# Optimization experiments

Measured on AMD Instinct MI355X. Metric: run time of the kernel, lower is better.

## Reference

```python
import jax, jax.numpy as jnp
import numpy as np

N = 524288   # total graph nodes
V = 64       # number of virtual nodes (clusters)
C = N // V   # nodes per cluster (8192)
D = 256      # in_feats
H = 256      # hidden_feats
EPS = 1e-5


def setup_inputs() -> dict:
    key = jax.random.key(0)
    ks = jax.random.split(key, 8)
    sD = 1.0 / np.sqrt(D)
    sH = 1.0 / np.sqrt(2 * H)
    inp = {
        "x": jax.random.normal(ks[0], (N, D), dtype=jnp.float32),
        "vn_emb": jax.random.normal(ks[1], (V, D), dtype=jnp.float32) * 0.1,
        "wq": jax.random.normal(ks[2], (D, D), dtype=jnp.float32) * sD,
        "wk": jax.random.normal(ks[3], (D, D), dtype=jnp.float32) * sD,
        "v_attn": jax.random.normal(ks[4], (D,), dtype=jnp.float32) * sD,
        "w1": jax.random.normal(ks[5], (D, 2 * H), dtype=jnp.float32) * sD,
        "b1": jnp.zeros((2 * H,), dtype=jnp.float32),
        "g1": jnp.ones((2 * H,), dtype=jnp.float32),
        "beta1": jnp.zeros((2 * H,), dtype=jnp.float32),
        "w2": jax.random.normal(ks[6], (2 * H, H), dtype=jnp.float32) * sH,
        "b2": jnp.zeros((H,), dtype=jnp.float32),
        "g2": jnp.ones((H,), dtype=jnp.float32),
        "beta2": jnp.zeros((H,), dtype=jnp.float32),
        # cluster v owns contiguous node block [v*C, (v+1)*C)
        "vn_index": jnp.arange(N, dtype=jnp.int32).reshape(V, C),
        "vn_indices": jnp.stack(
            [jnp.arange(N, dtype=jnp.int32), (jnp.arange(N, dtype=jnp.int32) // C)],
            axis=1),
    }
    return inp


def _batchnorm(z, g, b):
    # training-mode BN over the virtual-node batch dim
    m = jnp.mean(z, axis=0)
    v = jnp.var(z, axis=0)
    return (z - m) * jax.lax.rsqrt(v + EPS) * g + b


def reference(x, vn_emb, wq, wk, v_attn, w1, b1, g1, beta1,
              w2, b2, g2, beta2, vn_index, vn_indices):
    vx = vn_emb                                   # [V, D]
    # --- update_node_emb (layer 0): broadcast-add VN emb to its nodes ---
    h = x + vx[vn_indices[:, 1]]                  # [N, D]
    # --- update_vn_emb: per-cluster additive attention pooling (vectorized over V) ---
    cluster_h = h[vn_index]                       # [V, C, D]
    q = vx @ wq                                   # [V, D]
    kproj = jnp.einsum('vcd,de->vce', cluster_h, wk)   # [V, C, D]
    scores = jnp.einsum('vce,e->vc', jnp.tanh(kproj + q[:, None, :]), v_attn)
    attn = jax.nn.softmax(scores, axis=-1)        # [V, C]
    pooled = jnp.einsum('vc,vcd->vd', attn, cluster_h) + vx  # [V, D]
    # --- mlp_vns[0]: Linear -> BN -> ReLU -> Linear -> BN -> ReLU ---
    z = jax.nn.relu(_batchnorm(pooled @ w1 + b1, g1, beta1))  # [V, 2H]
    vx_new = jax.nn.relu(_batchnorm(z @ w2 + b2, g2, beta2))  # [V, H]
    return h, vx_new
```

## Files before the change

### kernel.cpp

```cpp
#include <hip/hip_runtime.h>


typedef __bf16 bf16x8 __attribute__((ext_vector_type(8)));
typedef float f32x4 __attribute__((ext_vector_type(4)));
typedef unsigned short us8 __attribute__((ext_vector_type(8)));

__device__ __forceinline__ unsigned short f2bf(float f) {
  unsigned int u = __float_as_uint(f);
  return (unsigned short)((u + 0x7fffu + ((u >> 16) & 1u)) >> 16);
}
__device__ __forceinline__ float bf2f(unsigned short s) {
  return __uint_as_float(((unsigned int)s) << 16);
}
__device__ __forceinline__ float tanh_fast(float x) {
  float cx = fminf(fmaxf(x, -15.f), 15.f);
  float e = __expf(2.f * cx);
  return (e - 1.f) * __builtin_amdgcn_rcpf(e + 1.f);
}
__device__ __forceinline__ float wave_sum(float v) {
#pragma unroll
  for (int o = 1; o < 64; o <<= 1) v += __shfl_xor(v, o);
  return v;
}
__device__ __forceinline__ void lgkm_barrier() {
  asm volatile("s_waitcnt lgkmcnt(0)" ::: "memory");
  __builtin_amdgcn_sched_barrier(0);
  __builtin_amdgcn_s_barrier();
  __builtin_amdgcn_sched_barrier(0);
}

__global__ __launch_bounds__(256) void k_prep(
    const float* __restrict__ vn_emb, const float* __restrict__ wq,
    const float* __restrict__ wk, float* __restrict__ qg,
    unsigned short* __restrict__ wkp) {
  int t = threadIdx.x;
  int b = blockIdx.x;
  if (b < 64) {
    float a = 0.f;
#pragma unroll 4
    for (int d = 0; d < 256; ++d) a += vn_emb[(b << 8) + d] * wq[(d << 8) + t];
    qg[(b << 8) + t] = a;
  } else {
    int tid = ((b - 64) << 8) + t;
    int l = tid & 63;
    int ks = (tid >> 6) & 7;
    int ct = tid >> 9;
    int col = (ct << 4) + (l & 15);
    int d0 = (ks << 5) + ((l >> 4) << 3);
    us8 o;
#pragma unroll
    for (int e = 0; e < 8; ++e) o[e] = f2bf(wk[(d0 + e) * 256 + col]);
    *reinterpret_cast<us8*>(wkp + (size_t)tid * 8) = o;
  }
}

__global__ __launch_bounds__(256, 4) void k_main(
    const float* __restrict__ x, const float* __restrict__ vn_emb,
    const float* __restrict__ v_attn, const float* __restrict__ qg,
    const unsigned short* __restrict__ wkp, float* __restrict__ hout,
    float* __restrict__ vecs, float* __restrict__ Zb) {
  __shared__ unsigned short hs[64 * 256];
  __shared__ float vxs[256], qv[256], va[256];

  const int t = threadIdx.x;
  const int blk = blockIdx.x;
  const int cl = blk >> 4;

  vxs[t] = vn_emb[(cl << 8) + t];
  qv[t] = qg[(cl << 8) + t];
  va[t] = v_attn[t];
  __syncthreads();

  const int l = t & 63, wv = t >> 6;
  const int lr = l & 15, lg = l >> 4;

  const float4* xv = reinterpret_cast<const float4*>(x);
  float4* ho = reinterpret_cast<float4*>(hout);
  char* hsb = reinterpret_cast<char*>(hs);
  const size_t base = (size_t)blk << 15;

  f32x4 acc = {0.f, 0.f, 0.f, 0.f};
  float zacc = 0.f;

  for (int sub = 0; sub < 8; ++sub) {
    const size_t sbase = base + ((size_t)sub << 12);

#pragma unroll 8
    for (int i = 0; i < 16; ++i) {
      int id = (i << 8) + t;
      float4 xx = xv[sbase + id];
      int row = id >> 6;
      int c4 = id & 63;
      const float4 vv = *reinterpret_cast<const float4*>(&vxs[c4 << 2]);
      float4 hh;
      hh.x = xx.x + vv.x;
      hh.y = xx.y + vv.y;
      hh.z = xx.z + vv.z;
      hh.w = xx.w + vv.w;
      ho[sbase + id] = hh;
      ushort4 o;
      o.x = f2bf(hh.x);
      o.y = f2bf(hh.y);
      o.z = f2bf(hh.z);
      o.w = f2bf(hh.w);
      int boff = (row << 9) + (((c4 << 3)) ^ ((row & 7) << 4));
      *reinterpret_cast<ushort4*>(hsb + boff) = o;
    }
    lgkm_barrier();

    bf16x8 bfr[8];
    {
      int row = (wv << 4) + lr;
      int sw = (row & 7) << 4;
#pragma unroll
      for (int ks = 0; ks < 8; ++ks) {
        int boff = (row << 9) + (((ks << 6) + (lg << 4)) ^ sw);
        bfr[ks] = __builtin_bit_cast(
            bf16x8, *reinterpret_cast<const us8*>(hsb + boff));
      }
    }
    float sp = 0.f;
    for (int ct = 0; ct < 16; ++ct) {
      f32x4 ac0 = {0.f, 0.f, 0.f, 0.f};
#pragma unroll
      for (int ks = 0; ks < 8; ++ks) {
        bf16x8 af = __builtin_bit_cast(
            bf16x8, *reinterpret_cast<const us8*>(
                        wkp + ((size_t)(((ct << 3) + ks) << 6) + l) * 8));
        ac0 =
            __builtin_amdgcn_mfma_f32_16x16x32_bf16(af, bfr[ks], ac0, 0, 0, 0);
      }
      const int eo0 = (ct << 4) + (lg << 2);
#pragma unroll
      for (int r = 0; r < 4; ++r)
        sp += tanh_fast(ac0[r] + qv[eo0 + r]) * va[eo0 + r];
    }
    sp += __shfl_xor(sp, 16);
    sp += __shfl_xor(sp, 32);
    float wgt = __expf(sp);
    zacc += wgt;

#pragma unroll
    for (int n = 0; n < 16; ++n) {
      float wn = __shfl(wgt, n);
      int row = (wv << 4) + n;
      int boff = (row << 9) + (((l << 3)) ^ ((row & 7) << 4));
      ushort4 hv = *reinterpret_cast<const ushort4*>(hsb + boff);
      acc[0] += wn * bf2f(hv.x);
      acc[1] += wn * bf2f(hv.y);
      acc[2] += wn * bf2f(hv.z);
      acc[3] += wn * bf2f(hv.w);
    }
    lgkm_barrier();
  }

  float zsum = wave_sum(zacc) * 0.25f;
  if (l == 0) va[wv] = zsum;
  float* sc = reinterpret_cast<float*>(hs);
  *reinterpret_cast<f32x4*>(&sc[(wv << 8) + (l << 2)]) = acc;
  __syncthreads();
  vecs[((size_t)blk << 8) + t] =
      sc[t] + sc[256 + t] + sc[512 + t] + sc[768 + t];
  if (t == 0) Zb[blk] = va[0] + va[1] + va[2] + va[3];
}

__global__ __launch_bounds__(256) void k_combine(
    const float* __restrict__ vecs, const float* __restrict__ Zb,
    const float* __restrict__ vn_emb, float* __restrict__ pooledT) {
  int v = blockIdx.x, t = threadIdx.x;
  float s = 0.f, z = 0.f;
#pragma unroll
  for (int b = 0; b < 16; ++b) {
    s += vecs[(size_t)(((v << 4) + b) << 8) + t];
    z += Zb[(v << 4) + b];
  }
  pooledT[(t << 6) + v] = s / z + vn_emb[(v << 8) + t];
}

__global__ __launch_bounds__(64) void k_mlp1(
    const float* __restrict__ pooledT, const float* __restrict__ w1,
    const float* __restrict__ b1, const float* __restrict__ g1,
    const float* __restrict__ be1, float* __restrict__ z1T) {
  int j = blockIdx.x, v = threadIdx.x;
  float a = 0.f;
#pragma unroll 4
  for (int d = 0; d < 256; ++d) a += pooledT[(d << 6) + v] * w1[(d << 9) + j];
  a += b1[j];
  float mu = wave_sum(a) * (1.f / 64.f);
  float df = a - mu;
  float var = wave_sum(df * df) * (1.f / 64.f);
  float z = df * rsqrtf(var + 1e-5f) * g1[j] + be1[j];
  z1T[(j << 6) + v] = fmaxf(z, 0.f);
}

__global__ __launch_bounds__(64) void k_mlp2(
    const float* __restrict__ z1T, const float* __restrict__ w2,
    const float* __restrict__ b2, const float* __restrict__ g2,
    const float* __restrict__ be2, float* __restrict__ vout) {
  int j = blockIdx.x, v = threadIdx.x;
  float a = 0.f;
#pragma unroll 4
  for (int k = 0; k < 512; ++k) a += z1T[(k << 6) + v] * w2[(k << 8) + j];
  a += b2[j];
  float mu = wave_sum(a) * (1.f / 64.f);
  float df = a - mu;
  float var = wave_sum(df * df) * (1.f / 64.f);
  float z = df * rsqrtf(var + 1e-5f) * g2[j] + be2[j];
  vout[(v << 8) + j] = fmaxf(z, 0.f);
}

extern "C" void kernel_launch(void* const* d_in, const int* in_sizes, int n_in,
                              void* d_out, int out_size, void* d_ws,
                              size_t ws_size, hipStream_t stream) {
  const float* x = (const float*)d_in[0];
  const float* vn_emb = (const float*)d_in[1];
  const float* wq = (const float*)d_in[2];
  const float* wk = (const float*)d_in[3];
  const float* v_attn = (const float*)d_in[4];
  const float* w1 = (const float*)d_in[5];
  const float* b1 = (const float*)d_in[6];
  const float* g1 = (const float*)d_in[7];
  const float* beta1 = (const float*)d_in[8];
  const float* w2 = (const float*)d_in[9];
  const float* b2 = (const float*)d_in[10];
  const float* g2 = (const float*)d_in[11];
  const float* beta2 = (const float*)d_in[12];

  char* wsb = (char*)d_ws;
  float* qg = (float*)(wsb + 0);
  unsigned short* wkp = (unsigned short*)(wsb + 65536);
  float* vecs = (float*)(wsb + 196608);
  float* Zb = (float*)(wsb + 1245184);
  float* pooledT = (float*)(wsb + 1249280);
  float* z1T = (float*)(wsb + 1314816);

  float* hout = (float*)d_out;
  float* vout = hout + (size_t)524288 * 256;

  k_prep<<<96, 256, 0, stream>>>(vn_emb, wq, wk, qg, wkp);
  k_main<<<1024, 256, 0, stream>>>(x, vn_emb, v_attn, qg, wkp, hout, vecs, Zb);
  k_combine<<<64, 256, 0, stream>>>(vecs, Zb, vn_emb, pooledT);
  k_mlp1<<<512, 64, 0, stream>>>(pooledT, w1, b1, g1, beta1, z1T);
  k_mlp2<<<256, 64, 0, stream>>>(z1T, w2, b2, g2, beta2, vout);
}
```

Before: 389.8 us.

## Give each wave a private LDS tile to drop block barriers in main loop

After: 539.0 us. +38.3%, slower.

```diff
diff --git a/kernel.cpp b/kernel.cpp
--- a/kernel.cpp
+++ b/kernel.cpp
@@ -21,12 +21,6 @@
 #pragma unroll
   for (int o = 1; o < 64; o <<= 1) v += __shfl_xor(v, o);
   return v;
-}
-__device__ __forceinline__ void lgkm_barrier() {
-  asm volatile("s_waitcnt lgkmcnt(0)" ::: "memory");
-  __builtin_amdgcn_sched_barrier(0);
-  __builtin_amdgcn_s_barrier();
-  __builtin_amdgcn_sched_barrier(0);
 }
 
 __global__ __launch_bounds__(256) void k_prep(
@@ -54,12 +48,12 @@
   }
 }
 
-__global__ __launch_bounds__(256, 4) void k_main(
+__global__ __launch_bounds__(256, 3) void k_hs(
     const float* __restrict__ x, const float* __restrict__ vn_emb,
     const float* __restrict__ v_attn, const float* __restrict__ qg,
     const unsigned short* __restrict__ wkp, float* __restrict__ hout,
     float* __restrict__ vecs, float* __restrict__ Zb) {
-  __shared__ unsigned short hs[64 * 256];
+  __shared__ unsigned short hs[4][16 * 256];
   __shared__ float vxs[256], qv[256], va[256];
 
   const int t = threadIdx.x;
@@ -74,93 +68,85 @@
   const int l = t & 63, wv = t >> 6;
   const int lr = l & 15, lg = l >> 4;
 
-  const float4* xv = reinterpret_cast<const float4*>(x);
-  float4* ho = reinterpret_cast<float4*>(hout);
-  char* hsb = reinterpret_cast<char*>(hs);
-  const size_t base = (size_t)blk << 15;
+  char* myhs = reinterpret_cast<char*>(hs[wv]);
+  const f32x4 vv = *reinterpret_cast<const f32x4*>(&vxs[l << 2]);
 
   f32x4 acc = {0.f, 0.f, 0.f, 0.f};
   float zacc = 0.f;
 
-  for (int sub = 0; sub < 8; ++sub) {
-    const size_t sbase = base + ((size_t)sub << 12);
-
-#pragma unroll 8
+  const size_t wrow0 = ((size_t)blk << 9) + ((size_t)wv << 7);
+
+  for (int chunk = 0; chunk < 8; ++chunk) {
+    const size_t row0 = wrow0 + ((size_t)chunk << 4);
+
+#pragma unroll
     for (int i = 0; i < 16; ++i) {
-      int id = (i << 8) + t;
-      float4 xx = xv[sbase + id];
-      int row = id >> 6;
-      int c4 = id & 63;
-      const float4 vv = *reinterpret_cast<const float4*>(&vxs[c4 << 2]);
-      float4 hh;
-      hh.x = xx.x + vv.x;
-      hh.y = xx.y + vv.y;
-      hh.z = xx.z + vv.z;
-      hh.w = xx.w + vv.w;
-      ho[sbase + id] = hh;
+      const size_t gidx = ((row0 + i) << 8) + (l << 2);
+      f32x4 xr = *reinterpret_cast<const f32x4*>(&x[gidx]);
+      f32x4 hh = xr + vv;
+      *reinterpret_cast<f32x4*>(&hout[gidx]) = hh;
       ushort4 o;
-      o.x = f2bf(hh.x);
-      o.y = f2bf(hh.y);
-      o.z = f2bf(hh.z);
-      o.w = f2bf(hh.w);
-      int boff = (row << 9) + (((c4 << 3)) ^ ((row & 7) << 4));
-      *reinterpret_cast<ushort4*>(hsb + boff) = o;
-    }
-    lgkm_barrier();
+      o.x = f2bf(hh[0]);
+      o.y = f2bf(hh[1]);
+      o.z = f2bf(hh[2]);
+      o.w = f2bf(hh[3]);
+      *reinterpret_cast<ushort4*>(
+          myhs + ((i << 9) + ((l << 3) ^ ((i & 7) << 4)))) = o;
+    }
+    asm volatile("s_waitcnt lgkmcnt(0)" ::: "memory");
+    __builtin_amdgcn_sched_barrier(0);
 
     bf16x8 bfr[8];
     {
-      int row = (wv << 4) + lr;
-      int sw = (row & 7) << 4;
-#pragma unroll
-      for (int ks = 0; ks < 8; ++ks) {
-        int boff = (row << 9) + (((ks << 6) + (lg << 4)) ^ sw);
+      const int sw = (lr & 7) << 4;
+#pragma unroll
+      for (int ks = 0; ks < 8; ++ks)
         bfr[ks] = __builtin_bit_cast(
-            bf16x8, *reinterpret_cast<const us8*>(hsb + boff));
-      }
-    }
+            bf16x8, *reinterpret_cast<const us8*>(
+                        myhs + ((lr << 9) + ((((ks << 6) + (lg << 4))) ^ sw))));
+    }
+
     float sp = 0.f;
+#pragma unroll 4
     for (int ct = 0; ct < 16; ++ct) {
       f32x4 ac0 = {0.f, 0.f, 0.f, 0.f};
 #pragma unroll
       for (int ks = 0; ks < 8; ++ks) {
         bf16x8 af = __builtin_bit_cast(
             bf16x8, *reinterpret_cast<const us8*>(
-                        wkp + ((size_t)(((ct << 3) + ks) << 6) + l) * 8));
-        ac0 =
-            __builtin_amdgcn_mfma_f32_16x16x32_bf16(af, bfr[ks], ac0, 0, 0, 0);
+                        wkp + ((size_t)((((ct << 3) + ks) << 6) + l)) * 8));
+        ac0 = __builtin_amdgcn_mfma_f32_16x16x32_bf16(af, bfr[ks], ac0, 0, 0, 0);
       }
       const int eo0 = (ct << 4) + (lg << 2);
-#pragma unroll
-      for (int r = 0; r < 4; ++r)
-        sp += tanh_fast(ac0[r] + qv[eo0 + r]) * va[eo0 + r];
+      const f32x4 qf = *reinterpret_cast<const f32x4*>(&qv[eo0]);
+      const f32x4 vf = *reinterpret_cast<const f32x4*>(&va[eo0]);
+#pragma unroll
+      for (int r = 0; r < 4; ++r) sp += tanh_fast(ac0[r] + qf[r]) * vf[r];
     }
     sp += __shfl_xor(sp, 16);
     sp += __shfl_xor(sp, 32);
-    float wgt = __expf(sp);
-    zacc += wgt;
+    float w = __expf(sp);
+    zacc += w;
 
 #pragma unroll
     for (int n = 0; n < 16; ++n) {
-      float wn = __shfl(wgt, n);
-      int row = (wv << 4) + n;
-      int boff = (row << 9) + (((l << 3)) ^ ((row & 7) << 4));
-      ushort4 hv = *reinterpret_cast<const ushort4*>(hsb + boff);
+      float wn = __shfl(w, n);
+      ushort4 hv = *reinterpret_cast<const ushort4*>(
+          myhs + ((n << 9) + ((l << 3) ^ ((n & 7) << 4))));
       acc[0] += wn * bf2f(hv.x);
       acc[1] += wn * bf2f(hv.y);
       acc[2] += wn * bf2f(hv.z);
       acc[3] += wn * bf2f(hv.w);
     }
-    lgkm_barrier();
   }
 
+  __syncthreads();
+  float* sc = reinterpret_cast<float*>(hs);
+  *reinterpret_cast<f32x4*>(&sc[(wv << 8) + (l << 2)]) = acc;
   float zsum = wave_sum(zacc) * 0.25f;
   if (l == 0) va[wv] = zsum;
-  float* sc = reinterpret_cast<float*>(hs);
-  *reinterpret_cast<f32x4*>(&sc[(wv << 8) + (l << 2)]) = acc;
   __syncthreads();
-  vecs[((size_t)blk << 8) + t] =
-      sc[t] + sc[256 + t] + sc[512 + t] + sc[768 + t];
+  vecs[((size_t)blk << 8) + t] = sc[t] + sc[256 + t] + sc[512 + t] + sc[768 + t];
   if (t == 0) Zb[blk] = va[0] + va[1] + va[2] + va[3];
 }
 
@@ -238,7 +224,7 @@
   float* vout = hout + (size_t)524288 * 256;
 
   k_prep<<<96, 256, 0, stream>>>(vn_emb, wq, wk, qg, wkp);
-  k_main<<<1024, 256, 0, stream>>>(x, vn_emb, v_attn, qg, wkp, hout, vecs, Zb);
+  k_hs<<<1024, 256, 0, stream>>>(x, vn_emb, v_attn, qg, wkp, hout, vecs, Zb);
   k_combine<<<64, 256, 0, stream>>>(vecs, Zb, vn_emb, pooledT);
   k_mlp1<<<512, 64, 0, stream>>>(pooledT, w1, b1, g1, beta1, z1T);
   k_mlp2<<<256, 64, 0, stream>>>(z1T, w2, b2, g2, beta2, vout);
```
